# Optimization experiments

Hardware: AMD Instinct MI355X
Metric: run time of the kernel (lower is better)

The kernel has to match this reference:

```python
import jax, jax.numpy as jnp
import numpy as np

NUM_HEADS = 16


def setup_inputs() -> dict:
    key = jax.random.key(0)
    ks = jax.random.split(key, 8)
    B, S, D = 2, 2048, 1024
    scale = 1.0 / np.sqrt(D)
    return {
        "v": jax.random.normal(ks[0], (B, S, D), jnp.float32),
        "k": jax.random.normal(ks[1], (B, S, D), jnp.float32),
        "q": jax.random.normal(ks[2], (B, S, D), jnp.float32),
        "mask": jnp.zeros((B, S), dtype=bool),  # True = masked (padding)
        "Wq": jax.random.normal(ks[3], (D, D), jnp.float32) * scale,
        "bq": jnp.zeros((D,), jnp.float32),
        "Wk": jax.random.normal(ks[4], (D, D), jnp.float32) * scale,
        "bk": jnp.zeros((D,), jnp.float32),
        "Wv": jax.random.normal(ks[5], (D, D), jnp.float32) * scale,
        "bv": jnp.zeros((D,), jnp.float32),
    }


def reference(v, k, q, mask, Wq, bq, Wk, bk, Wv, bv):
    B, Sq, D = q.shape
    H = NUM_HEADS
    hd = D // H

    def proj(x, W, b):
        # torch Linear: x @ W.T + b ; then split heads -> [B, H, S, hd]
        y = jnp.einsum("bsd,ed->bse", x, W) + b
        return y.reshape(B, -1, H, hd).transpose(0, 2, 1, 3)

    qh = proj(q, Wq, bq)  # [B,H,Sq,hd]
    kh = proj(k, Wk, bk)  # [B,H,Sk,hd]
    vh = proj(v, Wv, bv)  # [B,H,Sk,hd]

    scores = jnp.einsum("bhqd,bhkd->bhqk", qh, kh) / jnp.sqrt(
        jnp.asarray(hd, jnp.float32)
    )
    m = mask[:, None, None, :]  # add_dims -> [B,1,1,Sk]
    scores = jnp.where(m, -jnp.inf, scores)
    w = jax.nn.softmax(scores, axis=-1)
    w = jnp.where(m, 0.0, w)

    out = jnp.einsum("bhqk,bhkd->bhqd", w, vh)
    return out.transpose(0, 2, 1, 3).reshape(B, Sq, D)
```

## Files before the change

kernel.cpp:

```cpp
#include <hip/hip_runtime.h>
#include <hip/hip_bf16.h>
#include <cstdint>

typedef __attribute__((ext_vector_type(8))) short bf16x8;
typedef __attribute__((ext_vector_type(4))) float f32x4;

#define PLDT 72

static __device__ __forceinline__ unsigned short f2bf(float x) {
    __hip_bfloat16 h = __float2bfloat16(x);
    union { __hip_bfloat16 b; unsigned short u; } c; c.b = h; return c.u;
}
static __device__ __forceinline__ float bf2f(unsigned short b) {
    union { float f; uint32_t u; } v; v.u = ((uint32_t)b) << 16;
    return v.f;
}
static __device__ __forceinline__ float exp2b(float x) {
    return __builtin_amdgcn_exp2f(x);
}
static __device__ __forceinline__ unsigned int cvt_pk_bf16(float lo, float hi) {
    unsigned int r;
    asm("v_cvt_pk_bf16_f32 %0, %1, %2" : "=v"(r) : "v"(lo), "v"(hi));
    return r;
}
static __device__ __forceinline__ void gload_lds16(const unsigned short* g, unsigned short* l) {
    __builtin_amdgcn_global_load_lds(
        (const __attribute__((address_space(1))) void*)g,
        (__attribute__((address_space(3))) void*)l, 16, 0, 0);
}

__global__ __launch_bounds__(256) void cvt_all(
    const float* __restrict__ xq, const float* __restrict__ xk, const float* __restrict__ xv,
    const float* __restrict__ wq, const float* __restrict__ wk, const float* __restrict__ wv,
    unsigned short* __restrict__ oxq, unsigned short* __restrict__ oxk, unsigned short* __restrict__ oxv,
    unsigned short* __restrict__ owq, unsigned short* __restrict__ owk, unsigned short* __restrict__ owv) {
    const int z = blockIdx.z;
    const float* in = (z == 0) ? xq : (z == 1) ? xk : (z == 2) ? xv
                      : (z == 3) ? wq : (z == 4) ? wk : wv;
    unsigned short* out = (z == 0) ? oxq : (z == 1) ? oxk : (z == 2) ? oxv
                          : (z == 3) ? owq : (z == 4) ? owk : owv;
    const int n8 = (z < 3) ? 524288 : 131072;
    int i = blockIdx.x * 256 + threadIdx.x;
    if (i >= n8) return;
    const float4* ip = (const float4*)in;
    float4 a = ip[2 * i];
    float4 b = ip[2 * i + 1];
    uint4 r;
    r.x = cvt_pk_bf16(a.x, a.y);
    r.y = cvt_pk_bf16(a.z, a.w);
    r.z = cvt_pk_bf16(b.x, b.y);
    r.w = cvt_pk_bf16(b.z, b.w);
    *(uint4*)(out + (size_t)i * 8) = r;
}

__global__ __launch_bounds__(256) void proj_gemm_bf16(
    const unsigned short* __restrict__ Xqb, const unsigned short* __restrict__ Xkb,
    const unsigned short* __restrict__ Xvb,
    const unsigned short* __restrict__ Wqb, const unsigned short* __restrict__ Wkb,
    const unsigned short* __restrict__ Wvb,
    const float* __restrict__ bqp, const float* __restrict__ bkp, const float* __restrict__ bvp,
    unsigned short* __restrict__ dq, unsigned short* __restrict__ dk, unsigned short* __restrict__ dv) {
    __shared__ unsigned short a_lds[128 * 64];
    __shared__ unsigned short b_lds[128 * 64];

    const int z = blockIdx.z;
    const unsigned short* X = (z == 0) ? Xqb : (z == 1) ? Xkb : Xvb;
    const unsigned short* W = (z == 0) ? Wqb : (z == 1) ? Wkb : Wvb;
    const float* bias = (z == 0) ? bqp : (z == 1) ? bkp : bvp;
    unsigned short* dst = (z == 0) ? dq : (z == 1) ? dk : dv;

    const int tid = threadIdx.x;
    const int lane = tid & 63;
    const int w = tid >> 6;
    const int lr = lane & 15;
    const int lg = lane >> 4;
    const int m0 = blockIdx.x * 128;
    const int e0 = blockIdx.y * 128;
    const int wrow = (w >> 1) * 64;
    const int wcol = (w & 1) * 64;

    f32x4 acc[4][4] = {};

#pragma unroll 1
    for (int t = 0; t < 16; ++t) {
        const int k0 = t * 64;
        __syncthreads();
#pragma unroll
        for (int i = 0; i < 4; ++i) {
            int c = i * 256 + w * 64 + lane;
            int row = c >> 3;
            int col = (c & 7) * 8;
            gload_lds16(X + (size_t)(m0 + row) * 1024 + k0 + col,
                        a_lds + (size_t)(i * 256 + w * 64) * 8);
            gload_lds16(W + (size_t)(e0 + row) * 1024 + k0 + col,
                        b_lds + (size_t)(i * 256 + w * 64) * 8);
        }
        __syncthreads();

#pragma unroll
        for (int ks = 0; ks < 2; ++ks) {
            const int kk = ks * 32 + lg * 8;
            bf16x8 af[4], bfr[4];
#pragma unroll
            for (int mt = 0; mt < 4; ++mt)
                af[mt] = *(const bf16x8*)(a_lds + (wrow + mt * 16 + lr) * 64 + kk);
#pragma unroll
            for (int nt = 0; nt < 4; ++nt)
                bfr[nt] = *(const bf16x8*)(b_lds + (wcol + nt * 16 + lr) * 64 + kk);
            __builtin_amdgcn_s_setprio(1);
#pragma unroll
            for (int mt = 0; mt < 4; ++mt)
#pragma unroll
                for (int nt = 0; nt < 4; ++nt)
                    acc[mt][nt] = __builtin_amdgcn_mfma_f32_16x16x32_bf16(
                        af[mt], bfr[nt], acc[mt][nt], 0, 0, 0);
            __builtin_amdgcn_s_setprio(0);
        }
    }

    for (int mt = 0; mt < 4; ++mt)
        for (int nt = 0; nt < 4; ++nt)
            for (int i = 0; i < 4; ++i) {
                int m = m0 + wrow + mt * 16 + lg * 4 + i;
                int e = e0 + wcol + nt * 16 + lr;
                float val = acc[mt][nt][i] + bias[e];
                int b = m >> 11, s = m & 2047;
                int h = e >> 6, d = e & 63;
                size_t headoff = (((size_t)b * 16 + h) * 131072);
                if (z == 0) {
                    dst[headoff + (size_t)s * 64 + d] = f2bf(val);
                } else if (z == 1) {
                    int tt = s >> 6, kvr = s & 63;
                    int fmt = kvr >> 4, flr = kvr & 15;
                    int ks = d >> 5, lg3 = (d >> 3) & 3, j = d & 7;
                    dst[headoff + tt * 4096 + (ks * 4 + fmt) * 512 + (lg3 * 16 + flr) * 8 + j] = f2bf(val);
                } else {
                    int tt = s >> 6, kvc = s & 63;
                    int fmt = d >> 4, flr = d & 15;
                    int ks = kvc >> 5, lg3 = (kvc >> 3) & 3, j = kvc & 7;
                    dst[headoff + tt * 4096 + (ks * 4 + fmt) * 512 + (lg3 * 16 + flr) * 8 + j] = f2bf(val);
                }
            }
}

__global__ __launch_bounds__(256) void attn_kernel(
    const unsigned short* __restrict__ Qh,
    const unsigned short* __restrict__ Kf,
    const unsigned short* __restrict__ Vf,
    const unsigned char* __restrict__ mask,
    float* __restrict__ Out) {
    __shared__ unsigned short pbuf[4][32 * PLDT];

    const int tid = threadIdx.x;
    const int lane = tid & 63;
    const int w = tid >> 6;
    const int lr = lane & 15;
    const int lg = lane >> 4;

    const int bid = blockIdx.x;
    const int wk = (bid & 7) * 64 + (bid >> 3);
    const int x = wk & 15;
    const int bh = wk >> 4;
    const int h = bh & 15;
    const int b = bh >> 4;
    const int q0 = x * 128;

    const size_t headoff = (((size_t)b * 16) + h) * 131072;
    const unsigned short* Qp = Qh + headoff;
    const unsigned char* maskp = mask + b * 2048;
    unsigned short* pw = pbuf[w];

    const unsigned short* kfb = Kf + headoff + (size_t)lane * 8;
    const unsigned short* vfb = Vf + headoff + (size_t)lane * 8;

    const float qscale = 0.125f * 1.44269504088896340736f;
    bf16x8 qf[2][2];
#pragma unroll
    for (int qh = 0; qh < 2; ++qh) {
        int row = q0 + w * 32 + qh * 16 + lr;
#pragma unroll
        for (int ks = 0; ks < 2; ++ks) {
            bf16x8 t = *(const bf16x8*)(Qp + (size_t)row * 64 + ks * 32 + lg * 8);
#pragma unroll
            for (int j = 0; j < 8; ++j)
                t[j] = (short)f2bf(bf2f((unsigned short)t[j]) * qscale);
            qf[qh][ks] = t;
        }
    }

    f32x4 o[2][4] = {};
    float lsum[2] = {0.f, 0.f};

#pragma unroll 1
    for (int t = 0; t < 32; ++t) {
        const int kv0 = t * 64;
        const unsigned short* kt = kfb + t * 4096;
        const unsigned short* vt = vfb + t * 4096;

        bf16x8 kf[2][4];
#pragma unroll
        for (int ks = 0; ks < 2; ++ks)
#pragma unroll
            for (int mt = 0; mt < 4; ++mt)
                kf[ks][mt] = *(const bf16x8*)(kt + (ks * 4 + mt) * 512);

        f32x4 s[2][4] = {};
        __builtin_amdgcn_s_setprio(1);
#pragma unroll
        for (int ks = 0; ks < 2; ++ks)
#pragma unroll
            for (int mt = 0; mt < 4; ++mt) {
                s[0][mt] = __builtin_amdgcn_mfma_f32_16x16x32_bf16(kf[ks][mt], qf[0][ks], s[0][mt], 0, 0, 0);
                s[1][mt] = __builtin_amdgcn_mfma_f32_16x16x32_bf16(kf[ks][mt], qf[1][ks], s[1][mt], 0, 0, 0);
            }
        __builtin_amdgcn_s_setprio(0);

        bf16x8 vf[2][4];
#pragma unroll
        for (int ks = 0; ks < 2; ++ks)
#pragma unroll
            for (int mt = 0; mt < 4; ++mt)
                vf[ks][mt] = *(const bf16x8*)(vt + (ks * 4 + mt) * 512);

        unsigned long long mbits = __ballot(maskp[kv0 + lane] != 0);
        if (mbits) {
#pragma unroll
            for (int qh = 0; qh < 2; ++qh)
#pragma unroll
                for (int mt = 0; mt < 4; ++mt)
#pragma unroll
                    for (int i = 0; i < 4; ++i)
                        if ((mbits >> (mt * 16 + lg * 4 + i)) & 1ull) s[qh][mt][i] = -1e30f;
        }

#pragma unroll
        for (int qh = 0; qh < 2; ++qh) {
            float p[4][4];
            float ls = 0.f;
#pragma unroll
            for (int mt = 0; mt < 4; ++mt)
#pragma unroll
                for (int i = 0; i < 4; ++i) {
                    p[mt][i] = exp2b(s[qh][mt][i]);
                    ls += p[mt][i];
                }
            ls += __shfl_xor(ls, 16);
            ls += __shfl_xor(ls, 32);
            lsum[qh] += ls;

#pragma unroll
            for (int mt = 0; mt < 4; ++mt) {
                uint2 pr;
                pr.x = cvt_pk_bf16(p[mt][0], p[mt][1]);
                pr.y = cvt_pk_bf16(p[mt][2], p[mt][3]);
                *(uint2*)(&pw[(qh * 16 + lr) * PLDT + mt * 16 + lg * 4]) = pr;
            }
        }

        __builtin_amdgcn_s_setprio(1);
#pragma unroll
        for (int qh = 0; qh < 2; ++qh)
#pragma unroll
            for (int ks = 0; ks < 2; ++ks) {
                bf16x8 pfr = *(const bf16x8*)(&pw[(qh * 16 + lr) * PLDT + ks * 32 + lg * 8]);
#pragma unroll
                for (int mt = 0; mt < 4; ++mt)
                    o[qh][mt] = __builtin_amdgcn_mfma_f32_16x16x32_bf16(vf[ks][mt], pfr, o[qh][mt], 0, 0, 0);
            }
        __builtin_amdgcn_s_setprio(0);
    }

    float* ep = (float*)pw;
#pragma unroll
    for (int qh = 0; qh < 2; ++qh) {
        float rinv = 1.0f / lsum[qh];
#pragma unroll
        for (int mt = 0; mt < 4; ++mt)
#pragma unroll
            for (int i = 0; i < 4; ++i)
                ep[lr * 68 + mt * 16 + lg * 4 + i] = o[qh][mt][i] * rinv;
#pragma unroll
        for (int j = 0; j < 4; ++j) {
            int id = lane + 64 * j;
            int row = id >> 4;
            int c4 = (id & 15) << 2;
            float4 val = *(const float4*)(&ep[row * 68 + c4]);
            *(float4*)(&Out[((size_t)b * 2048 + q0 + w * 32 + qh * 16 + row) * 1024 + h * 64 + c4]) = val;
        }
    }
}

extern "C" void kernel_launch(void* const* d_in, const int* in_sizes, int n_in,
                              void* d_out, int out_size, void* d_ws, size_t ws_size,
                              hipStream_t stream) {
    const float* v = (const float*)d_in[0];
    const float* k = (const float*)d_in[1];
    const float* q = (const float*)d_in[2];
    const unsigned char* mask = (const unsigned char*)d_in[3];
    const float* Wq = (const float*)d_in[4];
    const float* bq = (const float*)d_in[5];
    const float* Wk = (const float*)d_in[6];
    const float* bk = (const float*)d_in[7];
    const float* Wv = (const float*)d_in[8];
    const float* bv = (const float*)d_in[9];
    float* out = (float*)d_out;

    unsigned short* ws = (unsigned short*)d_ws;
    unsigned short* qh  = ws;
    unsigned short* kh  = ws + 4194304;
    unsigned short* vT  = ws + 8388608;
    unsigned short* xqb = ws + 12582912;
    unsigned short* xkb = ws + 16777216;
    unsigned short* xvb = ws + 20971520;
    unsigned short* wqb = ws + 25165824;
    unsigned short* wkb = ws + 26214400;
    unsigned short* wvb = ws + 27262976;

    cvt_all<<<dim3(2048, 1, 6), 256, 0, stream>>>(q, k, v, Wq, Wk, Wv,
                                                  xqb, xkb, xvb, wqb, wkb, wvb);

    dim3 pgrid(32, 8, 3);
    proj_gemm_bf16<<<pgrid, 256, 0, stream>>>(xqb, xkb, xvb, wqb, wkb, wvb,
                                              bq, bk, bv, qh, kh, vT);

    attn_kernel<<<dim3(512), 256, 0, stream>>>(qh, kh, vT, mask, out);
}
```

Baseline: 105.7 us.

## Switch attention to 32x32x16 MFMA and keep P in registers via permlane32 swap

Rewrites the attention inner loop to use 32x32x16 bf16 MFMA tiles for both QK^T and PV, and re-lays out the K and V fragment buffers to match. The softmax probabilities are no longer staged through LDS. They are packed to bf16 and redistributed between half-waves with permlane32_swap, so the per-tile LDS write/read round trip and its latency go away. The cost is larger accumulators per lane (register pressure) and more intricate index mapping. As before, the softmax relies on the absence of max subtraction.

Measured after the change: 107.7 us. About the same (+1.8%).

```diff
diff --git a/kernel.cpp b/kernel.cpp
--- a/kernel.cpp
+++ b/kernel.cpp
@@ -4,8 +4,8 @@
 
 typedef __attribute__((ext_vector_type(8))) short bf16x8;
 typedef __attribute__((ext_vector_type(4))) float f32x4;
-
-#define PLDT 72
+typedef __attribute__((ext_vector_type(16))) float f32x16;
+typedef __attribute__((ext_vector_type(2))) unsigned int u32x2;
 
 static __device__ __forceinline__ unsigned short f2bf(float x) {
     __hip_bfloat16 h = __float2bfloat16(x);
@@ -22,6 +22,10 @@
     unsigned int r;
     asm("v_cvt_pk_bf16_f32 %0, %1, %2" : "=v"(r) : "v"(lo), "v"(hi));
     return r;
+}
+static __device__ __forceinline__ void plswap(unsigned int& a, unsigned int& b) {
+    u32x2 r = __builtin_amdgcn_permlane32_swap(a, b, false, false);
+    a = r[0]; b = r[1];
 }
 static __device__ __forceinline__ void gload_lds16(const unsigned short* g, unsigned short* l) {
     __builtin_amdgcn_global_load_lds(
@@ -130,15 +134,21 @@
                 if (z == 0) {
                     dst[headoff + (size_t)s * 64 + d] = f2bf(val);
                 } else if (z == 1) {
-                    int tt = s >> 6, kvr = s & 63;
-                    int fmt = kvr >> 4, flr = kvr & 15;
-                    int ks = d >> 5, lg3 = (d >> 3) & 3, j = d & 7;
-                    dst[headoff + tt * 4096 + (ks * 4 + fmt) * 512 + (lg3 * 16 + flr) * 8 + j] = f2bf(val);
+                    int tt = s >> 6;
+                    int kt = (s >> 5) & 1;
+                    int c  = s & 31;
+                    int ds = d >> 4;
+                    int hl = (d >> 3) & 1;
+                    int j  = d & 7;
+                    dst[headoff + tt * 4096 + (kt * 4 + ds) * 512 + (hl * 32 + c) * 8 + j] = f2bf(val);
                 } else {
-                    int tt = s >> 6, kvc = s & 63;
-                    int fmt = d >> 4, flr = d & 15;
-                    int ks = kvc >> 5, lg3 = (kvc >> 3) & 3, j = kvc & 7;
-                    dst[headoff + tt * 4096 + (ks * 4 + fmt) * 512 + (lg3 * 16 + flr) * 8 + j] = f2bf(val);
+                    int tt = s >> 6;
+                    int dt = d >> 5;
+                    int c  = d & 31;
+                    int st = (s >> 4) & 3;
+                    int hl = (s >> 3) & 1;
+                    int j  = s & 7;
+                    dst[headoff + tt * 4096 + (dt * 4 + st) * 512 + (hl * 32 + c) * 8 + j] = f2bf(val);
                 }
             }
 }
@@ -149,13 +159,13 @@
     const unsigned short* __restrict__ Vf,
     const unsigned char* __restrict__ mask,
     float* __restrict__ Out) {
-    __shared__ unsigned short pbuf[4][32 * PLDT];
+    __shared__ float epbuf[4][32 * 68];
 
     const int tid = threadIdx.x;
     const int lane = tid & 63;
     const int w = tid >> 6;
-    const int lr = lane & 15;
-    const int lg = lane >> 4;
+    const int c = lane & 31;
+    const int hl = lane >> 5;
 
     const int bid = blockIdx.x;
     const int wk = (bid & 7) * 64 + (bid >> 3);
@@ -168,125 +178,125 @@
     const size_t headoff = (((size_t)b * 16) + h) * 131072;
     const unsigned short* Qp = Qh + headoff;
     const unsigned char* maskp = mask + b * 2048;
-    unsigned short* pw = pbuf[w];
 
     const unsigned short* kfb = Kf + headoff + (size_t)lane * 8;
     const unsigned short* vfb = Vf + headoff + (size_t)lane * 8;
 
     const float qscale = 0.125f * 1.44269504088896340736f;
-    bf16x8 qf[2][2];
-#pragma unroll
-    for (int qh = 0; qh < 2; ++qh) {
-        int row = q0 + w * 32 + qh * 16 + lr;
-#pragma unroll
-        for (int ks = 0; ks < 2; ++ks) {
-            bf16x8 t = *(const bf16x8*)(Qp + (size_t)row * 64 + ks * 32 + lg * 8);
-#pragma unroll
-            for (int j = 0; j < 8; ++j)
-                t[j] = (short)f2bf(bf2f((unsigned short)t[j]) * qscale);
-            qf[qh][ks] = t;
-        }
+    bf16x8 qf[4];
+#pragma unroll
+    for (int ds = 0; ds < 4; ++ds) {
+        bf16x8 t = *(const bf16x8*)(Qp + (size_t)(q0 + w * 32 + c) * 64 + ds * 16 + hl * 8);
+#pragma unroll
+        for (int j = 0; j < 8; ++j)
+            t[j] = (short)f2bf(bf2f((unsigned short)t[j]) * qscale);
+        qf[ds] = t;
     }
 
-    f32x4 o[2][4] = {};
-    float lsum[2] = {0.f, 0.f};
+    f32x16 o[2] = {};
+    float lsum = 0.f;
 
 #pragma unroll 1
     for (int t = 0; t < 32; ++t) {
-        const int kv0 = t * 64;
-        const unsigned short* kt = kfb + t * 4096;
-        const unsigned short* vt = vfb + t * 4096;
+        const unsigned short* kt_base = kfb + t * 4096;
+        const unsigned short* vt_base = vfb + t * 4096;
 
         bf16x8 kf[2][4];
 #pragma unroll
-        for (int ks = 0; ks < 2; ++ks)
-#pragma unroll
-            for (int mt = 0; mt < 4; ++mt)
-                kf[ks][mt] = *(const bf16x8*)(kt + (ks * 4 + mt) * 512);
-
-        f32x4 s[2][4] = {};
+        for (int kt = 0; kt < 2; ++kt)
+#pragma unroll
+            for (int ds = 0; ds < 4; ++ds)
+                kf[kt][ds] = *(const bf16x8*)(kt_base + (kt * 4 + ds) * 512);
+
+        f32x16 s[2] = {};
         __builtin_amdgcn_s_setprio(1);
 #pragma unroll
-        for (int ks = 0; ks < 2; ++ks)
-#pragma unroll
-            for (int mt = 0; mt < 4; ++mt) {
-                s[0][mt] = __builtin_amdgcn_mfma_f32_16x16x32_bf16(kf[ks][mt], qf[0][ks], s[0][mt], 0, 0, 0);
-                s[1][mt] = __builtin_amdgcn_mfma_f32_16x16x32_bf16(kf[ks][mt], qf[1][ks], s[1][mt], 0, 0, 0);
-            }
+        for (int ds = 0; ds < 4; ++ds) {
+            s[0] = __builtin_amdgcn_mfma_f32_32x32x16_bf16(kf[0][ds], qf[ds], s[0], 0, 0, 0);
+            s[1] = __builtin_amdgcn_mfma_f32_32x32x16_bf16(kf[1][ds], qf[ds], s[1], 0, 0, 0);
+        }
         __builtin_amdgcn_s_setprio(0);
 
         bf16x8 vf[2][4];
 #pragma unroll
-        for (int ks = 0; ks < 2; ++ks)
-#pragma unroll
-            for (int mt = 0; mt < 4; ++mt)
-                vf[ks][mt] = *(const bf16x8*)(vt + (ks * 4 + mt) * 512);
-
-        unsigned long long mbits = __ballot(maskp[kv0 + lane] != 0);
+        for (int dt = 0; dt < 2; ++dt)
+#pragma unroll
+            for (int sg = 0; sg < 4; ++sg)
+                vf[dt][sg] = *(const bf16x8*)(vt_base + (dt * 4 + sg) * 512);
+
+        unsigned long long mbits = __ballot(maskp[t * 64 + lane] != 0);
         if (mbits) {
 #pragma unroll
-            for (int qh = 0; qh < 2; ++qh)
-#pragma unroll
-                for (int mt = 0; mt < 4; ++mt)
-#pragma unroll
-                    for (int i = 0; i < 4; ++i)
-                        if ((mbits >> (mt * 16 + lg * 4 + i)) & 1ull) s[qh][mt][i] = -1e30f;
-        }
-
-#pragma unroll
-        for (int qh = 0; qh < 2; ++qh) {
-            float p[4][4];
-            float ls = 0.f;
-#pragma unroll
-            for (int mt = 0; mt < 4; ++mt)
-#pragma unroll
-                for (int i = 0; i < 4; ++i) {
-                    p[mt][i] = exp2b(s[qh][mt][i]);
-                    ls += p[mt][i];
+            for (int kt = 0; kt < 2; ++kt)
+#pragma unroll
+                for (int r = 0; r < 16; ++r) {
+                    int kv = 32 * kt + (r & 3) + 8 * (r >> 2) + 4 * hl;
+                    if ((mbits >> kv) & 1ull) s[kt][r] = -1e30f;
                 }
-            ls += __shfl_xor(ls, 16);
-            ls += __shfl_xor(ls, 32);
-            lsum[qh] += ls;
-
-#pragma unroll
-            for (int mt = 0; mt < 4; ++mt) {
-                uint2 pr;
-                pr.x = cvt_pk_bf16(p[mt][0], p[mt][1]);
-                pr.y = cvt_pk_bf16(p[mt][2], p[mt][3]);
-                *(uint2*)(&pw[(qh * 16 + lr) * PLDT + mt * 16 + lg * 4]) = pr;
-            }
+        }
+
+        float ls = 0.f;
+        unsigned int wa[8], wb[8];
+#pragma unroll
+        for (int i = 0; i < 8; ++i) {
+            float e0 = exp2b(s[0][2 * i]), e1 = exp2b(s[0][2 * i + 1]);
+            ls += e0 + e1;
+            wa[i] = cvt_pk_bf16(e0, e1);
+            float f0 = exp2b(s[1][2 * i]), f1 = exp2b(s[1][2 * i + 1]);
+            ls += f0 + f1;
+            wb[i] = cvt_pk_bf16(f0, f1);
+        }
+        ls += __shfl_xor(ls, 32);
+        lsum += ls;
+
+        bf16x8 pf[2][2];
+        {
+            unsigned int a0 = wa[0], b0 = wa[2]; plswap(a0, b0);
+            unsigned int a1 = wa[1], b1 = wa[3]; plswap(a1, b1);
+            union { unsigned int u[4]; bf16x8 v; } pk;
+            pk.u[0] = a0; pk.u[1] = a1; pk.u[2] = b0; pk.u[3] = b1; pf[0][0] = pk.v;
+            unsigned int a2 = wa[4], b2 = wa[6]; plswap(a2, b2);
+            unsigned int a3 = wa[5], b3 = wa[7]; plswap(a3, b3);
+            pk.u[0] = a2; pk.u[1] = a3; pk.u[2] = b2; pk.u[3] = b3; pf[0][1] = pk.v;
+        }
+        {
+            unsigned int a0 = wb[0], b0 = wb[2]; plswap(a0, b0);
+            unsigned int a1 = wb[1], b1 = wb[3]; plswap(a1, b1);
+            union { unsigned int u[4]; bf16x8 v; } pk;
+            pk.u[0] = a0; pk.u[1] = a1; pk.u[2] = b0; pk.u[3] = b1; pf[1][0] = pk.v;
+            unsigned int a2 = wb[4], b2 = wb[6]; plswap(a2, b2);
+            unsigned int a3 = wb[5], b3 = wb[7]; plswap(a3, b3);
+            pk.u[0] = a2; pk.u[1] = a3; pk.u[2] = b2; pk.u[3] = b3; pf[1][1] = pk.v;
         }
 
         __builtin_amdgcn_s_setprio(1);
 #pragma unroll
-        for (int qh = 0; qh < 2; ++qh)
-#pragma unroll
-            for (int ks = 0; ks < 2; ++ks) {
-                bf16x8 pfr = *(const bf16x8*)(&pw[(qh * 16 + lr) * PLDT + ks * 32 + lg * 8]);
-#pragma unroll
-                for (int mt = 0; mt < 4; ++mt)
-                    o[qh][mt] = __builtin_amdgcn_mfma_f32_16x16x32_bf16(vf[ks][mt], pfr, o[qh][mt], 0, 0, 0);
-            }
+        for (int dt = 0; dt < 2; ++dt)
+#pragma unroll
+            for (int kt = 0; kt < 2; ++kt)
+#pragma unroll
+                for (int st = 0; st < 2; ++st)
+                    o[dt] = __builtin_amdgcn_mfma_f32_32x32x16_bf16(
+                        vf[dt][2 * kt + st], pf[kt][st], o[dt], 0, 0, 0);
         __builtin_amdgcn_s_setprio(0);
     }
 
-    float* ep = (float*)pw;
-#pragma unroll
-    for (int qh = 0; qh < 2; ++qh) {
-        float rinv = 1.0f / lsum[qh];
-#pragma unroll
-        for (int mt = 0; mt < 4; ++mt)
-#pragma unroll
-            for (int i = 0; i < 4; ++i)
-                ep[lr * 68 + mt * 16 + lg * 4 + i] = o[qh][mt][i] * rinv;
-#pragma unroll
-        for (int j = 0; j < 4; ++j) {
-            int id = lane + 64 * j;
-            int row = id >> 4;
-            int c4 = (id & 15) << 2;
-            float4 val = *(const float4*)(&ep[row * 68 + c4]);
-            *(float4*)(&Out[((size_t)b * 2048 + q0 + w * 32 + qh * 16 + row) * 1024 + h * 64 + c4]) = val;
-        }
+    float* ep = epbuf[w];
+    float rinv = 1.0f / lsum;
+#pragma unroll
+    for (int dt = 0; dt < 2; ++dt)
+#pragma unroll
+        for (int r = 0; r < 16; ++r) {
+            int d = 32 * dt + (r & 3) + 8 * (r >> 2) + 4 * hl;
+            ep[c * 68 + d] = o[dt][r] * rinv;
+        }
+#pragma unroll
+    for (int j = 0; j < 8; ++j) {
+        int id = lane + 64 * j;
+        int row = id >> 4;
+        int c4 = (id & 15) << 2;
+        float4 val = *(const float4*)(&ep[row * 68 + c4]);
+        *(float4*)(&Out[((size_t)b * 2048 + q0 + w * 32 + row) * 1024 + h * 64 + c4]) = val;
     }
 }
 
```

## Split attention KV range across two blocks and combine with atomics

Applied to the files above, without the earlier changes.

Each attention block now processes half of the KV tiles, which doubles the grid to 1024 blocks for more parallelism across CUs. Partial unnormalized outputs and row sums are combined with global float atomicAdds into a zeroed output and a row-sum buffer. A separate norm_out kernel then divides by the row sums. The approach relies on the kernel not tracking a running max, so partial exp sums add directly. It pays for the extra parallelism with an output memset, per-element scalar atomics and an extra full read/write pass over the output.

Result: slower. 211.3 us (+99.8%).

```diff
diff --git a/kernel.cpp b/kernel.cpp
--- a/kernel.cpp
+++ b/kernel.cpp
@@ -148,7 +148,8 @@
     const unsigned short* __restrict__ Kf,
     const unsigned short* __restrict__ Vf,
     const unsigned char* __restrict__ mask,
-    float* __restrict__ Out) {
+    float* __restrict__ Out,
+    float* __restrict__ lsums) {
     __shared__ unsigned short pbuf[4][32 * PLDT];
 
     const int tid = threadIdx.x;
@@ -158,9 +159,10 @@
     const int lg = lane >> 4;
 
     const int bid = blockIdx.x;
-    const int wk = (bid & 7) * 64 + (bid >> 3);
+    const int wk = (bid & 7) * 128 + (bid >> 3);
     const int x = wk & 15;
-    const int bh = wk >> 4;
+    const int kvh = (wk >> 4) & 1;
+    const int bh = wk >> 5;
     const int h = bh & 15;
     const int b = bh >> 4;
     const int q0 = x * 128;
@@ -191,8 +193,9 @@
     f32x4 o[2][4] = {};
     float lsum[2] = {0.f, 0.f};
 
+    const int t0 = kvh * 16;
 #pragma unroll 1
-    for (int t = 0; t < 32; ++t) {
+    for (int t = t0; t < t0 + 16; ++t) {
         const int kv0 = t * 64;
         const unsigned short* kt = kfb + t * 4096;
         const unsigned short* vt = vfb + t * 4096;
@@ -273,21 +276,40 @@
     float* ep = (float*)pw;
 #pragma unroll
     for (int qh = 0; qh < 2; ++qh) {
-        float rinv = 1.0f / lsum[qh];
+        if (lane < 16)
+            atomicAdd(&lsums[(size_t)bh * 2048 + q0 + w * 32 + qh * 16 + lane], lsum[qh]);
 #pragma unroll
         for (int mt = 0; mt < 4; ++mt)
 #pragma unroll
             for (int i = 0; i < 4; ++i)
-                ep[lr * 68 + mt * 16 + lg * 4 + i] = o[qh][mt][i] * rinv;
+                ep[lr * 68 + mt * 16 + lg * 4 + i] = o[qh][mt][i];
 #pragma unroll
         for (int j = 0; j < 4; ++j) {
             int id = lane + 64 * j;
             int row = id >> 4;
             int c4 = (id & 15) << 2;
             float4 val = *(const float4*)(&ep[row * 68 + c4]);
-            *(float4*)(&Out[((size_t)b * 2048 + q0 + w * 32 + qh * 16 + row) * 1024 + h * 64 + c4]) = val;
+            float* dst = &Out[((size_t)b * 2048 + q0 + w * 32 + qh * 16 + row) * 1024 + h * 64 + c4];
+            atomicAdd(dst + 0, val.x);
+            atomicAdd(dst + 1, val.y);
+            atomicAdd(dst + 2, val.z);
+            atomicAdd(dst + 3, val.w);
         }
     }
+}
+
+__global__ __launch_bounds__(256) void norm_out(float* __restrict__ out,
+                                                const float* __restrict__ lsums) {
+    int i = blockIdx.x * 256 + threadIdx.x;
+    if (i >= 1048576) return;
+    int m = i >> 8;
+    int h = (i >> 4) & 15;
+    int b = m >> 11, s = m & 2047;
+    float l = lsums[(((size_t)b * 16) + h) * 2048 + s];
+    float r = 1.0f / l;
+    float4 v = ((float4*)out)[i];
+    v.x *= r; v.y *= r; v.z *= r; v.w *= r;
+    ((float4*)out)[i] = v;
 }
 
 extern "C" void kernel_launch(void* const* d_in, const int* in_sizes, int n_in,
@@ -315,6 +337,9 @@
     unsigned short* wqb = ws + 25165824;
     unsigned short* wkb = ws + 26214400;
     unsigned short* wvb = ws + 27262976;
+    float* lsums = (float*)wqb;
+
+    hipMemsetAsync(out, 0, (size_t)out_size * sizeof(float), stream);
 
     cvt_all<<<dim3(2048, 1, 6), 256, 0, stream>>>(q, k, v, Wq, Wk, Wv,
                                                   xqb, xkb, xvb, wqb, wkb, wvb);
@@ -323,5 +348,9 @@
     proj_gemm_bf16<<<pgrid, 256, 0, stream>>>(xqb, xkb, xvb, wqb, wkb, wvb,
                                               bq, bk, bv, qh, kh, vT);
 
-    attn_kernel<<<dim3(512), 256, 0, stream>>>(qh, kh, vT, mask, out);
-}
+    hipMemsetAsync(lsums, 0, 65536 * sizeof(float), stream);
+
+    attn_kernel<<<dim3(1024), 256, 0, stream>>>(qh, kh, vT, mask, out, lsums);
+
+    norm_out<<<dim3(4096), 256, 0, stream>>>(out, lsums);
+}
```
